# Performance work log

Measured on AMD Instinct MI355X. Metric: run time of the kernel, lower is better.

The kernel has to match this reference:

```python
import jax, jax.numpy as jnp
import numpy as np

# --- model dims (match init_kwargs) ---
B, N = 2, 4096          # batch, seq_len
D = 1024                # model dim
H, DH = 16, 64          # heads, dim_head (inner = H*DH = D)
R = 64                  # num_random_features
L = 6                   # depth
FF = 4 * D              # ff_dim
V = 32000               # vocab_size
MAXN = 4096             # max_seq_len
EPS = 1e-5              # torch LayerNorm default eps
STAB = 1e-6             # numerical_stabilizer
INNER = H * DH


def _ln(x, g, b):
    m = jnp.mean(x, axis=-1, keepdims=True)
    v = jnp.mean(jnp.square(x - m), axis=-1, keepdims=True)
    return (x - m) * jax.lax.rsqrt(v + EPS) * g + b


def setup_inputs() -> dict:
    key = jax.random.key(0)
    ks = jax.random.split(key, 16)
    s = 0.02
    return {
        "tokens": jax.random.randint(ks[0], (B, N), 0, V),
        "tok_emb": jax.random.normal(ks[1], (V, D), jnp.float32) * s,
        "pos_emb": jax.random.normal(ks[2], (MAXN, D), jnp.float32) * s,
        "Wqkv": jax.random.normal(ks[3], (L, 3 * INNER, D), jnp.float32) * s,
        "Wout": jax.random.normal(ks[4], (L, D, INNER), jnp.float32) * s,
        "bout": jnp.zeros((L, D), jnp.float32),
        "ln1_g": jnp.ones((L, D), jnp.float32),
        "ln1_b": jnp.zeros((L, D), jnp.float32),
        "ln2_g": jnp.ones((L, D), jnp.float32),
        "ln2_b": jnp.zeros((L, D), jnp.float32),
        "W1": jax.random.normal(ks[5], (L, FF, D), jnp.float32) * s,
        "b1": jnp.zeros((L, FF), jnp.float32),
        "W2": jax.random.normal(ks[6], (L, D, FF), jnp.float32) * s,
        "b2": jnp.zeros((L, D), jnp.float32),
        # random_features buffer: randn / sqrt(R)
        "rf": jax.random.normal(ks[7], (L, H, DH, R), jnp.float32) / np.sqrt(R),
    }


def reference(tokens, tok_emb, pos_emb, Wqkv, Wout, bout,
              ln1_g, ln1_b, ln2_g, ln2_b, W1, b1, W2, b2, rf):
    b, n = tokens.shape
    x = tok_emb[tokens] + pos_emb[jnp.arange(n)][None]  # [b,n,D]
    for l in range(L):
        # --- Performer attention (FAVOR+ linear path, ReLU kernel) ---
        h = _ln(x, ln1_g[l], ln1_b[l])
        qkv = h @ Wqkv[l].T                                  # [b,n,3*INNER]
        q, k, v = jnp.split(qkv, 3, axis=-1)
        resh = lambda t: t.reshape(b, n, H, DH).transpose(0, 2, 1, 3)  # [b,h,n,d]
        q, k, v = resh(q), resh(k), resh(v)
        phi_q = jax.nn.relu(jnp.einsum('bhnd,hdr->bhnr', q, rf[l]))
        phi_k = jax.nn.relu(jnp.einsum('bhnd,hdr->bhnr', k, rf[l]))
        kv = jnp.einsum('bhnr,bhnd->bhrd', phi_k, v)          # [b,h,r,d]
        out = jnp.einsum('bhnr,bhrd->bhnd', phi_q, kv)        # [b,h,n,d]
        # normalizer = phi_q . (sum_m phi_k)
        normz = jnp.einsum('bhnr,bhr->bhn', phi_q, phi_k.sum(axis=2))[..., None] + STAB
        out = out / normz
        out = out.transpose(0, 2, 1, 3).reshape(b, n, INNER)
        x = x + (out @ Wout[l].T + bout[l])
        # --- FFN (GELU exact, matching torch nn.GELU) ---
        h2 = _ln(x, ln2_g[l], ln2_b[l])
        ff = jax.nn.gelu(h2 @ W1[l].T + b1[l], approximate=False) @ W2[l].T + b2[l]
        x = x + ff
    return x
```

## Files before the change

kernel.cpp:

```cpp
#include <hip/hip_runtime.h>
#include <hip/hip_bf16.h>
#include <math.h>

#define NL 6
#define DMODEL 1024
#define NHEAD 16
#define MTOT 8192
#define NSEQ 4096
#define FFDIM 4096

typedef __attribute__((ext_vector_type(8))) short bf16x8;
typedef __attribute__((ext_vector_type(4))) short s16x4;
typedef __attribute__((ext_vector_type(4))) float f32x4;

__device__ __forceinline__ float b2f(short s) {
    unsigned int u = ((unsigned int)(unsigned short)s) << 16;
    return __uint_as_float(u);
}
__device__ __forceinline__ short f2b(float f) {
    __hip_bfloat16 h = __float2bfloat16(f);
    return *reinterpret_cast<short*>(&h);
}
__device__ __forceinline__ f32x4 mfma16(bf16x8 a, bf16x8 b, f32x4 c) {
    return __builtin_amdgcn_mfma_f32_16x16x32_bf16(a, b, c, 0, 0, 0);
}
__device__ __forceinline__ void gload16(const void* g, void* lds) {
    __builtin_amdgcn_global_load_lds((__attribute__((address_space(1))) void*)(g),
                                     (__attribute__((address_space(3))) void*)(lds), 16, 0, 0);
}

__global__ __launch_bounds__(256) void cvt_f2b_kernel(const float* __restrict__ in,
        short* __restrict__ out, int n4) {
    int i = blockIdx.x * 256 + threadIdx.x;
    if (i >= n4) return;
    float4 v = ((const float4*)in)[i];
    s16x4 o;
    o[0] = f2b(v.x); o[1] = f2b(v.y); o[2] = f2b(v.z); o[3] = f2b(v.w);
    ((s16x4*)out)[i] = o;
}

__global__ __launch_bounds__(256) void embed_kernel(const int* __restrict__ tok,
        const float* __restrict__ te, const float* __restrict__ pe, float* __restrict__ x) {
    int row = blockIdx.x, tid = threadIdx.x;
    int t = tok[row], n = row & (NSEQ - 1);
    float4 a = ((const float4*)(te + (size_t)t * DMODEL))[tid];
    float4 p = ((const float4*)(pe + (size_t)n * DMODEL))[tid];
    float4 o;
    o.x = a.x + p.x; o.y = a.y + p.y; o.z = a.z + p.z; o.w = a.w + p.w;
    ((float4*)(x + (size_t)row * DMODEL))[tid] = o;
}

__global__ __launch_bounds__(256) void prep_wcomb(const float* __restrict__ Wqkv,
        const float* __restrict__ rf, short* __restrict__ Wcomb) {
    int id = blockIdx.x;
    int l = id / 3072, row = id % 3072;
    int tid = threadIdx.x;
    size_t outbase = ((size_t)l * 3072 + row) * DMODEL;
    if (row >= 2048) {
        #pragma unroll
        for (int it = 0; it < 4; it++)
            Wcomb[outbase + it * 256 + tid] = f2b(Wqkv[outbase + it * 256 + tid]);
        return;
    }
    int base = (row < 1024) ? 0 : 1024;
    int hh = (row & 1023) >> 6, r = row & 63;
    __shared__ float rfl[64];
    if (tid < 64) rfl[tid] = rf[(((size_t)l * NHEAD + hh) * 64 + tid) * 64 + r];
    __syncthreads();
    #pragma unroll
    for (int it = 0; it < 4; it++) {
        int k = it * 256 + tid;
        float acc = 0.f;
        #pragma unroll 8
        for (int d = 0; d < 64; d++)
            acc += rfl[d] * Wqkv[((size_t)l * 3072 + base + hh * 64 + d) * DMODEL + k];
        Wcomb[outbase + k] = f2b(acc);
    }
}

__global__ __launch_bounds__(256) void ln_kernel(const float* __restrict__ x,
        const float* __restrict__ g, const float* __restrict__ bta, short* __restrict__ h) {
    int row = blockIdx.x, tid = threadIdx.x, lane = tid & 63, w = tid >> 6;
    float4 v = ((const float4*)(x + (size_t)row * DMODEL))[tid];
    float s = v.x + v.y + v.z + v.w;
    float sq = v.x * v.x + v.y * v.y + v.z * v.z + v.w * v.w;
    #pragma unroll
    for (int off = 32; off > 0; off >>= 1) { s += __shfl_down(s, off); sq += __shfl_down(sq, off); }
    __shared__ float ss[4], sqq[4];
    if (lane == 0) { ss[w] = s; sqq[w] = sq; }
    __syncthreads();
    float st = ss[0] + ss[1] + ss[2] + ss[3];
    float sqt = sqq[0] + sqq[1] + sqq[2] + sqq[3];
    float mean = st * (1.f / 1024.f);
    float var = sqt * (1.f / 1024.f) - mean * mean;
    float rstd = rsqrtf(var + 1e-5f);
    int col = tid * 4;
    float4 gg = ((const float4*)g)[tid];
    float4 bb = ((const float4*)bta)[tid];
    s16x4 o;
    o[0] = f2b((v.x - mean) * rstd * gg.x + bb.x);
    o[1] = f2b((v.y - mean) * rstd * gg.y + bb.y);
    o[2] = f2b((v.z - mean) * rstd * gg.z + bb.z);
    o[3] = f2b((v.w - mean) * rstd * gg.w + bb.w);
    *(s16x4*)&h[(size_t)row * DMODEL + col] = o;
}

#define EPI_QKV 0
#define EPI_BIASRES 1
#define EPI_GELU 2

template <int EPI>
__global__ __launch_bounds__(256) void gemm_bt(const short* __restrict__ A,
        const short* __restrict__ B, int K, int N,
        const float* __restrict__ bias, float* __restrict__ resx,
        short* __restrict__ out0, short* __restrict__ out1, short* __restrict__ out2) {
    __shared__ short As[128 * 32];
    __shared__ short Bs[128 * 32];
    const int tid = threadIdx.x;
    const int lane = tid & 63;
    const int w = tid >> 6;
    const int bn = blockIdx.x, bm = blockIdx.y;
    const int warow = (w >> 1) * 64;
    const int wacol = (w & 1) * 64;
    const int q = lane >> 4;

    f32x4 acc[4][4];
    #pragma unroll
    for (int i = 0; i < 4; i++)
        #pragma unroll
        for (int j = 0; j < 4; j++)
            #pragma unroll
            for (int c = 0; c < 4; c++) acc[i][j][c] = 0.f;

    const int s0 = tid, s1 = 256 + tid;
    const int rowA0 = s0 >> 2, rowA1 = s1 >> 2;
    const int j0 = (s0 & 3) ^ ((rowA0 >> 1) & 3);
    const int j1 = (s1 & 3) ^ ((rowA1 >> 1) & 3);
    const size_t aBase0 = (size_t)(bm * 128 + rowA0) * K + j0 * 8;
    const size_t aBase1 = (size_t)(bm * 128 + rowA1) * K + j1 * 8;
    const size_t bBase0 = (size_t)(bn * 128 + rowA0) * K + j0 * 8;
    const size_t bBase1 = (size_t)(bn * 128 + rowA1) * K + j1 * 8;
    short* ldsA0 = &As[(s0 & ~63) * 8];
    short* ldsA1 = &As[(s1 & ~63) * 8];
    short* ldsB0 = &Bs[(s0 & ~63) * 8];
    short* ldsB1 = &Bs[(s1 & ~63) * 8];

    for (int k0 = 0; k0 < K; k0 += 32) {
        gload16(A + aBase0 + k0, ldsA0);
        gload16(A + aBase1 + k0, ldsA1);
        gload16(B + bBase0 + k0, ldsB0);
        gload16(B + bBase1 + k0, ldsB1);
        __syncthreads();
        bf16x8 af[4], bfr[4];
        #pragma unroll
        for (int mt = 0; mt < 4; mt++) {
            int m = warow + mt * 16 + (lane & 15);
            int jj = q ^ ((m >> 1) & 3);
            af[mt] = *(const bf16x8*)&As[m * 32 + jj * 8];
        }
        #pragma unroll
        for (int nt = 0; nt < 4; nt++) {
            int n = wacol + nt * 16 + (lane & 15);
            int jj = q ^ ((n >> 1) & 3);
            bfr[nt] = *(const bf16x8*)&Bs[n * 32 + jj * 8];
        }
        #pragma unroll
        for (int mt = 0; mt < 4; mt++)
            #pragma unroll
            for (int nt = 0; nt < 4; nt++)
                acc[mt][nt] = mfma16(af[mt], bfr[nt], acc[mt][nt]);
        __syncthreads();
    }

    #pragma unroll
    for (int mt = 0; mt < 4; mt++) {
        int row0 = bm * 128 + warow + mt * 16 + (q << 2);
        #pragma unroll
        for (int nt = 0; nt < 4; nt++) {
            int col = bn * 128 + wacol + nt * 16 + (lane & 15);
            f32x4 v = acc[mt][nt];
            if (EPI == EPI_QKV) {
                if (col < 1024) {
                    #pragma unroll
                    for (int i = 0; i < 4; i++)
                        out0[(size_t)(row0 + i) * DMODEL + col] = f2b(fmaxf(v[i], 0.f));
                } else if (col < 2048) {
                    int c = col - 1024, hh = c >> 6, r = c & 63;
                    int b = row0 >> 12, n0 = row0 & (NSEQ - 1);
                    s16x4 pk;
                    #pragma unroll
                    for (int i = 0; i < 4; i++) pk[i] = f2b(fmaxf(v[i], 0.f));
                    *(s16x4*)&out1[((size_t)((b * NHEAD + hh) * 64 + r)) * NSEQ + n0] = pk;
                } else {
                    int c = col - 2048, hh = c >> 6, dd = c & 63;
                    int b = row0 >> 12, n0 = row0 & (NSEQ - 1);
                    s16x4 pk;
                    #pragma unroll
                    for (int i = 0; i < 4; i++) pk[i] = f2b(v[i]);
                    *(s16x4*)&out2[((size_t)((b * NHEAD + hh) * 64 + dd)) * NSEQ + n0] = pk;
                }
            } else if (EPI == EPI_BIASRES) {
                float bb = bias[col];
                #pragma unroll
                for (int i = 0; i < 4; i++) {
                    size_t idx = (size_t)(row0 + i) * N + col;
                    resx[idx] += v[i] + bb;
                }
            } else {
                float bb = bias[col];
                #pragma unroll
                for (int i = 0; i < 4; i++) {
                    float t = v[i] + bb;
                    float gg = 0.5f * t * (1.f + erff(t * 0.70710678118654752f));
                    out0[(size_t)(row0 + i) * N + col] = f2b(gg);
                }
            }
        }
    }
}

__global__ __launch_bounds__(256) void zero_kvs(float* kvs) {
    int i = blockIdx.x * 256 + threadIdx.x;
    if (i < 32 * 65 * 64) kvs[i] = 0.f;
}

__global__ __launch_bounds__(256) void kv_kernel(const short* __restrict__ phiKT,
        const short* __restrict__ vT, float* __restrict__ kvs) {
    int bh = blockIdx.x;
    int kc = blockIdx.y;
    int tid = threadIdx.x, lane = tid & 63, w = tid >> 6, q = lane >> 4;
    f32x4 acc[4];
    #pragma unroll
    for (int nt = 0; nt < 4; nt++)
        #pragma unroll
        for (int c = 0; c < 4; c++) acc[nt][c] = 0.f;
    const short* Abase = vT + ((size_t)(bh * 64 + w * 16 + (lane & 15))) * NSEQ;
    for (int ks = 0; ks < 16; ks++) {
        int k0 = kc * 512 + ks * 32 + q * 8;
        bf16x8 a = *(const bf16x8*)&Abase[k0];
        #pragma unroll
        for (int nt = 0; nt < 4; nt++) {
            bf16x8 b = *(const bf16x8*)&phiKT[((size_t)(bh * 64 + nt * 16 + (lane & 15))) * NSEQ + k0];
            acc[nt] = mfma16(a, b, acc[nt]);
        }
    }
    #pragma unroll
    for (int nt = 0; nt < 4; nt++)
        #pragma unroll
        for (int i = 0; i < 4; i++)
            atomicAdd(&kvs[((size_t)bh * 65 + (w * 16 + q * 4 + i)) * 64 + nt * 16 + (lane & 15)],
                      acc[nt][i]);
    int r = tid & 63, qq = tid >> 6;
    const short* p = phiKT + ((size_t)(bh * 64 + r)) * NSEQ + kc * 512 + qq * 128;
    float s = 0.f;
    #pragma unroll 8
    for (int u = 0; u < 128; u++) s += b2f(p[u]);
    __shared__ float red[256];
    red[tid] = s;
    __syncthreads();
    if (tid < 64) {
        float t = red[tid] + red[tid + 64] + red[tid + 128] + red[tid + 192];
        atomicAdd(&kvs[((size_t)bh * 65 + 64) * 64 + tid], t);
    }
}

__global__ __launch_bounds__(256) void cvt_kvs(const float* __restrict__ kvs,
        short* __restrict__ kvsb) {
    int bh = blockIdx.x, tid = threadIdx.x;
    for (int idx = tid; idx < 80 * 64; idx += 256) {
        int row = idx >> 6, col = idx & 63;
        float v = (row < 65) ? kvs[((size_t)bh * 65 + row) * 64 + col] : 0.f;
        kvsb[((size_t)bh * 80 + row) * 64 + col] = f2b(v);
    }
}

__global__ __launch_bounds__(256) void attn_kernel(const short* __restrict__ phiQ,
        const short* __restrict__ kvsb, short* __restrict__ attnO) {
    int mt = blockIdx.x;
    int bh = blockIdx.y;
    int b = bh >> 4, h = bh & 15;
    int tid = threadIdx.x, lane = tid & 63, w = tid >> 6, q = lane >> 4;
    int mrow = mt * 64 + w * 16 + (lane & 15);
    const short* Abase = phiQ + ((size_t)(b * NSEQ + mrow)) * DMODEL + h * 64;
    f32x4 acc[5];
    #pragma unroll
    for (int nt = 0; nt < 5; nt++)
        #pragma unroll
        for (int c = 0; c < 4; c++) acc[nt][c] = 0.f;
    #pragma unroll
    for (int k0 = 0; k0 < 64; k0 += 32) {
        bf16x8 a = *(const bf16x8*)&Abase[k0 + q * 8];
        #pragma unroll
        for (int nt = 0; nt < 5; nt++) {
            bf16x8 bb = *(const bf16x8*)&kvsb[((size_t)bh * 80 + nt * 16 + (lane & 15)) * 64 + k0 + q * 8];
            acc[nt] = mfma16(a, bb, acc[nt]);
        }
    }
    int n0 = mt * 64 + w * 16 + q * 4;
    #pragma unroll
    for (int i = 0; i < 4; i++) {
        float nz = __shfl(acc[4][i], (lane & 48)) + 1e-6f;
        #pragma unroll
        for (int nt = 0; nt < 4; nt++) {
            float val = acc[nt][i] / nz;
            attnO[((size_t)(b * NSEQ + n0 + i)) * DMODEL + h * 64 + nt * 16 + (lane & 15)] = f2b(val);
        }
    }
}

__global__ __launch_bounds__(256) void cvt_out(const float* __restrict__ x,
        float* __restrict__ out) {
    size_t i = (size_t)blockIdx.x * 256 + threadIdx.x;
    ((float4*)out)[i] = ((const float4*)x)[i];
}

extern "C" void kernel_launch(void* const* d_in, const int* in_sizes, int n_in,
                              void* d_out, int out_size, void* d_ws, size_t ws_size,
                              hipStream_t stream) {
    const int* tokens = (const int*)d_in[0];
    const float* tok_emb = (const float*)d_in[1];
    const float* pos_emb = (const float*)d_in[2];
    const float* Wqkv = (const float*)d_in[3];
    const float* Wout = (const float*)d_in[4];
    const float* bout = (const float*)d_in[5];
    const float* ln1g = (const float*)d_in[6];
    const float* ln1b = (const float*)d_in[7];
    const float* ln2g = (const float*)d_in[8];
    const float* ln2b = (const float*)d_in[9];
    const float* W1 = (const float*)d_in[10];
    const float* b1 = (const float*)d_in[11];
    const float* W2 = (const float*)d_in[12];
    const float* b2 = (const float*)d_in[13];
    const float* rf = (const float*)d_in[14];

    char* ws = (char*)d_ws;
    float* x      = (float*)ws;
    short* Wcomb  = (short*)(ws + 33554432);
    short* WoutB  = (short*)(ws + 71303168);
    short* W1B    = (short*)(ws + 83886080);
    short* W2B    = (short*)(ws + 134217728);
    short* h      = (short*)(ws + 184549376);
    short* phiQ   = (short*)(ws + 201326592);
    short* phiKT  = (short*)(ws + 218103808);
    short* vT     = (short*)(ws + 234881024);
    short* attnO  = (short*)(ws + 251658240);
    short* ff     = phiQ;
    float* kvs    = (float*)(ws + 268435456);
    short* kvsb   = (short*)(ws + 268967936);

    embed_kernel<<<MTOT, 256, 0, stream>>>(tokens, tok_emb, pos_emb, x);
    prep_wcomb<<<NL * 3072, 256, 0, stream>>>(Wqkv, rf, Wcomb);
    cvt_f2b_kernel<<<(NL * 1024 * 1024 / 4 + 255) / 256, 256, 0, stream>>>(Wout, WoutB, NL * 1024 * 1024 / 4);
    cvt_f2b_kernel<<<(NL * 4096 * 1024 / 4 + 255) / 256, 256, 0, stream>>>(W1, W1B, NL * 4096 * 1024 / 4);
    cvt_f2b_kernel<<<(NL * 1024 * 4096 / 4 + 255) / 256, 256, 0, stream>>>(W2, W2B, NL * 1024 * 4096 / 4);

    for (int l = 0; l < NL; l++) {
        ln_kernel<<<MTOT, 256, 0, stream>>>(x, ln1g + l * 1024, ln1b + l * 1024, h);
        gemm_bt<EPI_QKV><<<dim3(24, 64), 256, 0, stream>>>(
            h, Wcomb + (size_t)l * 3072 * 1024, 1024, 3072,
            nullptr, nullptr, phiQ, phiKT, vT);
        zero_kvs<<<520, 256, 0, stream>>>(kvs);
        kv_kernel<<<dim3(32, 8), 256, 0, stream>>>(phiKT, vT, kvs);
        cvt_kvs<<<32, 256, 0, stream>>>(kvs, kvsb);
        attn_kernel<<<dim3(64, 32), 256, 0, stream>>>(phiQ, kvsb, attnO);
        gemm_bt<EPI_BIASRES><<<dim3(8, 64), 256, 0, stream>>>(
            attnO, WoutB + (size_t)l * 1024 * 1024, 1024, 1024,
            bout + l * 1024, x, nullptr, nullptr, nullptr);
        ln_kernel<<<MTOT, 256, 0, stream>>>(x, ln2g + l * 1024, ln2b + l * 1024, h);
        gemm_bt<EPI_GELU><<<dim3(32, 64), 256, 0, stream>>>(
            h, W1B + (size_t)l * 4096 * 1024, 1024, 4096,
            b1 + l * 4096, nullptr, ff, nullptr, nullptr);
        gemm_bt<EPI_BIASRES><<<dim3(8, 64), 256, 0, stream>>>(
            ff, W2B + (size_t)l * 1024 * 4096, 4096, 1024,
            b2 + l * 1024, x, nullptr, nullptr, nullptr);
    }
    cvt_out<<<MTOT * DMODEL / 1024, 256, 0, stream>>>(x, (float*)d_out);
}
```

Before: 3.144 ms.

## Double GEMM K-tile to 64 and restructure weight-combination prep kernel

The bf16 GEMM now stages a 64-wide K slice per iteration with an 8-way XOR swizzle, halving the number of barrier pairs per K loop, and adds a 3-blocks-per-CU launch bound. The rf-folding prep kernel is rewritten so each thread computes 64 output rows for one column from an LDS-resident rf tile, with a separate vectorized conversion kernel for the V weights. The larger LDS footprint and the 64-float accumulator array raise register and LDS pressure, which may limit occupancy.

```diff
diff --git a/kernel.cpp b/kernel.cpp
--- a/kernel.cpp
+++ b/kernel.cpp
@@ -50,32 +50,53 @@
     ((float4*)(x + (size_t)row * DMODEL))[tid] = o;
 }
 
-__global__ __launch_bounds__(256) void prep_wcomb(const float* __restrict__ Wqkv,
+__global__ __launch_bounds__(256) void prep_phi(const float* __restrict__ Wqkv,
         const float* __restrict__ rf, short* __restrict__ Wcomb) {
-    int id = blockIdx.x;
-    int l = id / 3072, row = id % 3072;
+    int b = blockIdx.x;
+    int kc = b & 3, qk = (b >> 2) & 1, h = (b >> 3) & 15, l = b >> 7;
     int tid = threadIdx.x;
-    size_t outbase = ((size_t)l * 3072 + row) * DMODEL;
-    if (row >= 2048) {
-        #pragma unroll
-        for (int it = 0; it < 4; it++)
-            Wcomb[outbase + it * 256 + tid] = f2b(Wqkv[outbase + it * 256 + tid]);
-        return;
-    }
-    int base = (row < 1024) ? 0 : 1024;
-    int hh = (row & 1023) >> 6, r = row & 63;
-    __shared__ float rfl[64];
-    if (tid < 64) rfl[tid] = rf[(((size_t)l * NHEAD + hh) * 64 + tid) * 64 + r];
+    __shared__ float rfl[64 * 64];
+    const float* rfg = rf + ((size_t)(l * NHEAD + h)) * 4096;
+    #pragma unroll
+    for (int u = 0; u < 4; u++) {
+        int i4 = u * 256 + tid;
+        ((float4*)rfl)[i4] = ((const float4*)rfg)[i4];
+    }
     __syncthreads();
-    #pragma unroll
-    for (int it = 0; it < 4; it++) {
-        int k = it * 256 + tid;
-        float acc = 0.f;
-        #pragma unroll 8
-        for (int d = 0; d < 64; d++)
-            acc += rfl[d] * Wqkv[((size_t)l * 3072 + base + hh * 64 + d) * DMODEL + k];
-        Wcomb[outbase + k] = f2b(acc);
-    }
+    int k = kc * 256 + tid;
+    const float* wq = Wqkv + ((size_t)(l * 3072 + qk * 1024 + h * 64)) * DMODEL + k;
+    float acc[64];
+    #pragma unroll
+    for (int r = 0; r < 64; r++) acc[r] = 0.f;
+    #pragma unroll 4
+    for (int d = 0; d < 64; d++) {
+        float wd = wq[(size_t)d * DMODEL];
+        const float4* rrow = (const float4*)&rfl[d * 64];
+        #pragma unroll
+        for (int r4 = 0; r4 < 16; r4++) {
+            float4 f = rrow[r4];
+            acc[r4 * 4 + 0] += f.x * wd;
+            acc[r4 * 4 + 1] += f.y * wd;
+            acc[r4 * 4 + 2] += f.z * wd;
+            acc[r4 * 4 + 3] += f.w * wd;
+        }
+    }
+    size_t outbase = ((size_t)(l * 3072 + qk * 1024 + h * 64)) * DMODEL + k;
+    #pragma unroll
+    for (int r = 0; r < 64; r++)
+        Wcomb[outbase + (size_t)r * DMODEL] = f2b(acc[r]);
+}
+
+__global__ __launch_bounds__(256) void prep_v(const float* __restrict__ Wqkv,
+        short* __restrict__ Wcomb) {
+    int b = blockIdx.x;
+    int l = b >> 10, row = b & 1023;
+    int tid = threadIdx.x;
+    size_t base = ((size_t)(l * 3072 + 2048 + row)) * DMODEL;
+    float4 v = ((const float4*)(Wqkv + base))[tid];
+    s16x4 o;
+    o[0] = f2b(v.x); o[1] = f2b(v.y); o[2] = f2b(v.z); o[3] = f2b(v.w);
+    ((s16x4*)(Wcomb + base))[tid] = o;
 }
 
 __global__ __launch_bounds__(256) void ln_kernel(const float* __restrict__ x,
@@ -110,12 +131,12 @@
 #define EPI_GELU 2
 
 template <int EPI>
-__global__ __launch_bounds__(256) void gemm_bt(const short* __restrict__ A,
+__global__ __launch_bounds__(256, 3) void gemm_bt(const short* __restrict__ A,
         const short* __restrict__ B, int K, int N,
         const float* __restrict__ bias, float* __restrict__ resx,
         short* __restrict__ out0, short* __restrict__ out1, short* __restrict__ out2) {
-    __shared__ short As[128 * 32];
-    __shared__ short Bs[128 * 32];
+    __shared__ short As[128 * 64];
+    __shared__ short Bs[128 * 64];
     const int tid = threadIdx.x;
     const int lane = tid & 63;
     const int w = tid >> 6;
@@ -132,43 +153,47 @@
             #pragma unroll
             for (int c = 0; c < 4; c++) acc[i][j][c] = 0.f;
 
-    const int s0 = tid, s1 = 256 + tid;
-    const int rowA0 = s0 >> 2, rowA1 = s1 >> 2;
-    const int j0 = (s0 & 3) ^ ((rowA0 >> 1) & 3);
-    const int j1 = (s1 & 3) ^ ((rowA1 >> 1) & 3);
-    const size_t aBase0 = (size_t)(bm * 128 + rowA0) * K + j0 * 8;
-    const size_t aBase1 = (size_t)(bm * 128 + rowA1) * K + j1 * 8;
-    const size_t bBase0 = (size_t)(bn * 128 + rowA0) * K + j0 * 8;
-    const size_t bBase1 = (size_t)(bn * 128 + rowA1) * K + j1 * 8;
-    short* ldsA0 = &As[(s0 & ~63) * 8];
-    short* ldsA1 = &As[(s1 & ~63) * 8];
-    short* ldsB0 = &Bs[(s0 & ~63) * 8];
-    short* ldsB1 = &Bs[(s1 & ~63) * 8];
-
-    for (int k0 = 0; k0 < K; k0 += 32) {
-        gload16(A + aBase0 + k0, ldsA0);
-        gload16(A + aBase1 + k0, ldsA1);
-        gload16(B + bBase0 + k0, ldsB0);
-        gload16(B + bBase1 + k0, ldsB1);
+    unsigned aOff[4], bOff[4];
+    short* ldsA[4];
+    short* ldsB[4];
+    #pragma unroll
+    for (int i = 0; i < 4; i++) {
+        int s = i * 256 + tid;
+        int row = s >> 3, cp = s & 7;
+        int j = cp ^ ((row >> 1) & 7);
+        aOff[i] = (unsigned)((bm * 128 + row) * K + j * 8);
+        bOff[i] = (unsigned)((bn * 128 + row) * K + j * 8);
+        ldsA[i] = &As[s * 8];
+        ldsB[i] = &Bs[s * 8];
+    }
+
+    for (int k0 = 0; k0 < K; k0 += 64) {
+        #pragma unroll
+        for (int i = 0; i < 4; i++) gload16(A + aOff[i] + k0, ldsA[i]);
+        #pragma unroll
+        for (int i = 0; i < 4; i++) gload16(B + bOff[i] + k0, ldsB[i]);
         __syncthreads();
-        bf16x8 af[4], bfr[4];
-        #pragma unroll
-        for (int mt = 0; mt < 4; mt++) {
-            int m = warow + mt * 16 + (lane & 15);
-            int jj = q ^ ((m >> 1) & 3);
-            af[mt] = *(const bf16x8*)&As[m * 32 + jj * 8];
-        }
-        #pragma unroll
-        for (int nt = 0; nt < 4; nt++) {
-            int n = wacol + nt * 16 + (lane & 15);
-            int jj = q ^ ((n >> 1) & 3);
-            bfr[nt] = *(const bf16x8*)&Bs[n * 32 + jj * 8];
-        }
-        #pragma unroll
-        for (int mt = 0; mt < 4; mt++)
+        #pragma unroll
+        for (int ksub = 0; ksub < 2; ksub++) {
+            bf16x8 af[4], bfr[4];
             #pragma unroll
-            for (int nt = 0; nt < 4; nt++)
-                acc[mt][nt] = mfma16(af[mt], bfr[nt], acc[mt][nt]);
+            for (int mt = 0; mt < 4; mt++) {
+                int m = warow + mt * 16 + (lane & 15);
+                int c = (ksub * 4 + q) ^ ((m >> 1) & 7);
+                af[mt] = *(const bf16x8*)&As[m * 64 + c * 8];
+            }
+            #pragma unroll
+            for (int nt = 0; nt < 4; nt++) {
+                int n = wacol + nt * 16 + (lane & 15);
+                int c = (ksub * 4 + q) ^ ((n >> 1) & 7);
+                bfr[nt] = *(const bf16x8*)&Bs[n * 64 + c * 8];
+            }
+            #pragma unroll
+            for (int mt = 0; mt < 4; mt++)
+                #pragma unroll
+                for (int nt = 0; nt < 4; nt++)
+                    acc[mt][nt] = mfma16(af[mt], bfr[nt], acc[mt][nt]);
+        }
         __syncthreads();
     }
 
@@ -349,7 +374,8 @@
     short* kvsb   = (short*)(ws + 268967936);
 
     embed_kernel<<<MTOT, 256, 0, stream>>>(tokens, tok_emb, pos_emb, x);
-    prep_wcomb<<<NL * 3072, 256, 0, stream>>>(Wqkv, rf, Wcomb);
+    prep_phi<<<768, 256, 0, stream>>>(Wqkv, rf, Wcomb);
+    prep_v<<<NL * 1024, 256, 0, stream>>>(Wqkv, Wcomb);
     cvt_f2b_kernel<<<(NL * 1024 * 1024 / 4 + 255) / 256, 256, 0, stream>>>(Wout, WoutB, NL * 1024 * 1024 / 4);
     cvt_f2b_kernel<<<(NL * 4096 * 1024 / 4 + 255) / 256, 256, 0, stream>>>(W1, W1B, NL * 4096 * 1024 / 4);
     cvt_f2b_kernel<<<(NL * 1024 * 4096 / 4 + 255) / 256, 256, 0, stream>>>(W2, W2B, NL * 1024 * 4096 / 4);
```

After: 2.613 ms. 1.2x faster.
